# Performance work log

Hardware: AMD Instinct MI355X
Metric: run time of the kernel (lower is better)

## Reference

```python
import jax, jax.numpy as jnp
import numpy as np

N = 1_000_000
C = 64
H = Wd = 2048
EPS = 1e-5


def _build_neighbors(seed=0):
    """Active-site neighbor map for a 3x3 submanifold conv on an HxW grid.
    Returns int32 [N, 9]; entry = index of active neighbor site, or -1."""
    rng = np.random.default_rng(seed)
    flat = rng.permutation(H * Wd)[:N]            # unique active coords
    grid = np.full(H * Wd, -1, np.int64)
    grid[flat] = np.arange(N)
    ys, xs = flat // Wd, flat % Wd
    cols = []
    for dy in (-1, 0, 1):
        for dx in (-1, 0, 1):
            ny, nx = ys + dy, xs + dx
            valid = (ny >= 0) & (ny < H) & (nx >= 0) & (nx < Wd)
            nf = np.where(valid, np.clip(ny, 0, H - 1) * Wd + np.clip(nx, 0, Wd - 1), 0)
            nb = np.where(valid, grid[nf], -1)    # -1 also if neighbor inactive
            cols.append(nb)
    return np.stack(cols, axis=1).astype(np.int32)


def setup_inputs() -> dict:
    key = jax.random.key(0)
    k1, k2, k3 = jax.random.split(key, 3)
    scale = 1.0 / np.sqrt(9 * C)
    return {
        "features": jax.random.normal(k1, (N, C), jnp.float32),
        "neighbor": jnp.asarray(_build_neighbors()),
        "W1": jax.random.normal(k2, (9, C, C), jnp.float32) * scale,
        "gamma1": jnp.ones((C,), jnp.float32),
        "beta1": jnp.zeros((C,), jnp.float32),
        "W2": jax.random.normal(k3, (9, C, C), jnp.float32) * scale,
        "gamma2": jnp.ones((C,), jnp.float32),
        "beta2": jnp.zeros((C,), jnp.float32),
    }


def _subm_conv(f, W, neighbor):
    # gather -> per-tap GEMM -> accumulate (submanifold: outputs only at active sites)
    out = jnp.zeros_like(f)
    for k in range(9):
        idx = neighbor[:, k]
        mask = (idx >= 0)
        g = jnp.where(mask[:, None], f[jnp.maximum(idx, 0)], 0.0)  # [N, C]
        out = out + g @ W[k]
    return out


def _bn(f, gamma, beta):
    # BatchNorm1d over the active-site axis (training-mode batch statistics)
    m = f.mean(axis=0)
    v = f.var(axis=0)
    return (f - m) * jax.lax.rsqrt(v + EPS) * gamma + beta


def reference(features, neighbor, W1, gamma1, beta1, W2, gamma2, beta2):
    out = _subm_conv(features, W1, neighbor)
    out = jax.nn.relu(_bn(out, gamma1, beta1))
    out = _subm_conv(out, W2, neighbor)
    out = _bn(out, gamma2, beta2) + features
    return jax.nn.relu(out)
```

## Files before the change

kernel.cpp:

```cpp
#include <hip/hip_runtime.h>

#define NSITES 1000000
#define CCH 64
#define EPS_BN 1e-5f
#define INV_N (1.0f / 1000000.0f)

typedef __bf16 bf16x8 __attribute__((ext_vector_type(8)));
typedef float f32x4 __attribute__((ext_vector_type(4)));
typedef unsigned short ushort_t;

__device__ __forceinline__ unsigned short f2bf(float x) {
    __bf16 h = (__bf16)x;
    return __builtin_bit_cast(unsigned short, h);
}
__device__ __forceinline__ float bf2f(unsigned short u) {
    return (float)__builtin_bit_cast(__bf16, u);
}

__device__ __forceinline__ unsigned int actu32(unsigned int u, float a0, float b0,
                                               float a1, float b1) {
    float x0 = __builtin_bit_cast(float, u << 16);
    float x1 = __builtin_bit_cast(float, u & 0xffff0000u);
    float y0 = fmaxf(a0 * x0 + b0, 0.f);
    float y1 = fmaxf(a1 * x1 + b1, 0.f);
    return (unsigned int)f2bf(y0) | ((unsigned int)f2bf(y1) << 16);
}

__global__ void prep_kernel(const float* __restrict__ f, ushort_t* __restrict__ o,
                            const float* __restrict__ W1, const float* __restrict__ W2,
                            ushort_t* __restrict__ W1s, ushort_t* __restrict__ W2s,
                            float* __restrict__ stats, int total16) {
    int gtid = blockIdx.x * blockDim.x + threadIdx.x;
    if (gtid < 73728) {
        const float* Wg = W1;
        ushort_t* dst = W1s;
        int u = gtid;
        if (u >= 36864) { Wg = W2; dst = W2s; u -= 36864; }
        int j = u & 7;
        int lane = (u >> 3) & 63;
        int nt = (u >> 9) & 3;
        int kk = (u >> 11) & 1;
        int tap = u >> 12;
        int k = 32 * kk + 8 * (lane >> 4) + j;
        int n = 16 * nt + (lane & 15);
        dst[u] = f2bf(Wg[tap * 4096 + k * 64 + n]);
    } else if (gtid < 73984) {
        stats[gtid - 73728] = 0.f;
    } else if (gtid < 74016) {
        ((unsigned int*)(o + (size_t)NSITES * 64))[gtid - 73984] = 0u;
    }
    int stride = gridDim.x * blockDim.x;
    for (int i = gtid; i < total16; i += stride) {
        const float4* fp = (const float4*)(f + (size_t)i * 16);
        float4 v0 = fp[0];
        float4 v1 = fp[1];
        float4 v2 = fp[2];
        float4 v3 = fp[3];
        uint4 pa, pb;
        ushort_t* up = (ushort_t*)&pa;
        up[0] = f2bf(v0.x); up[1] = f2bf(v0.y); up[2] = f2bf(v0.z); up[3] = f2bf(v0.w);
        up[4] = f2bf(v1.x); up[5] = f2bf(v1.y); up[6] = f2bf(v1.z); up[7] = f2bf(v1.w);
        ushort_t* uq = (ushort_t*)&pb;
        uq[0] = f2bf(v2.x); uq[1] = f2bf(v2.y); uq[2] = f2bf(v2.z); uq[3] = f2bf(v2.w);
        uq[4] = f2bf(v3.x); uq[5] = f2bf(v3.y); uq[6] = f2bf(v3.z); uq[7] = f2bf(v3.w);
        uint4* op = (uint4*)(o + (size_t)i * 16);
        op[0] = pa;
        op[1] = pb;
    }
}

__device__ __forceinline__ void gatherA(const ushort_t* __restrict__ fin,
                                        const int (&idxr)[2][9], int t, int quad,
                                        uint4 (&dst)[2][2], int fallback) {
#pragma unroll
    for (int mt = 0; mt < 2; ++mt) {
        int id = idxr[mt][t];
        int r = (id < 0) ? fallback : id;
        const uint4* p = (const uint4*)(fin + ((size_t)r << 6) + (quad << 3));
        dst[mt][0] = p[0];
        dst[mt][1] = p[4];
    }
}

template <bool OUT_BF16, bool FUSE_ACT>
__global__ __launch_bounds__(256) void conv_kernel(
    const ushort_t* __restrict__ fin,
    const int* __restrict__ nbr,
    const ushort_t* __restrict__ Wsw,
    const float* __restrict__ p_sum, const float* __restrict__ p_sq,
    const float* __restrict__ p_gamma, const float* __restrict__ p_beta,
    ushort_t* __restrict__ out_bf, float* __restrict__ out_f,
    float* __restrict__ s_sum, float* __restrict__ s_sq) {

    __shared__ float bs_sum[64];
    __shared__ float bs_sq[64];
    __shared__ __align__(16) float s_a[64];
    __shared__ __align__(16) float s_b[64];

    const int tid  = threadIdx.x;
    const int wv   = tid >> 6;
    const int lane = tid & 63;
    const int quad = lane >> 4;
    const int l15  = lane & 15;
    const int sbase = blockIdx.x * 128 + wv * 32;

    if (tid < 64) {
        bs_sum[tid] = 0.f;
        bs_sq[tid] = 0.f;
        if constexpr (FUSE_ACT) {
            float m = p_sum[tid] * INV_N;
            float v = p_sq[tid] * INV_N - m * m;
            float s = p_gamma[tid] * rsqrtf(v + EPS_BN);
            s_a[tid] = s;
            s_b[tid] = p_beta[tid] - m * s;
        }
    }
    __syncthreads();

    float af[16], bfv[16];
    if constexpr (FUSE_ACT) {
#pragma unroll
        for (int j = 0; j < 8; ++j) {
            af[j]      = s_a[quad * 8 + j];
            af[8 + j]  = s_a[32 + quad * 8 + j];
            bfv[j]     = s_b[quad * 8 + j];
            bfv[8 + j] = s_b[32 + quad * 8 + j];
        }
    }

    int idxr[2][9];
#pragma unroll
    for (int mt = 0; mt < 2; ++mt) {
        int s = sbase + mt * 16 + l15;
        int sc = (s < NSITES) ? s : 0;
        bool sv = (s < NSITES);
#pragma unroll
        for (int t = 0; t < 9; ++t) {
            int id = nbr[(size_t)sc * 9 + t];
            idxr[mt][t] = sv ? id : -1;
        }
    }

    f32x4 acc[2][4];
#pragma unroll
    for (int mt = 0; mt < 2; ++mt)
#pragma unroll
        for (int nt = 0; nt < 4; ++nt) acc[mt][nt] = (f32x4){0.f, 0.f, 0.f, 0.f};

    constexpr int FB = FUSE_ACT ? 0 : NSITES;

    uint4 abuf[2][2][2];
    gatherA(fin, idxr, 0, quad, abuf[0], FB);

#pragma unroll
    for (int t = 0; t < 9; ++t) {
        bf16x8 B[2][4];
#pragma unroll
        for (int kk = 0; kk < 2; ++kk)
#pragma unroll
            for (int nt = 0; nt < 4; ++nt)
                B[kk][nt] = *(const bf16x8*)(Wsw + (size_t)(((t * 2 + kk) * 4 + nt) * 64 + lane) * 8);

        if (t < 8) gatherA(fin, idxr, t + 1, quad, abuf[(t + 1) & 1], FB);

        bf16x8 afr[2][2];
#pragma unroll
        for (int mt = 0; mt < 2; ++mt) {
            uint4 r0 = abuf[t & 1][mt][0];
            uint4 r1 = abuf[t & 1][mt][1];
            if constexpr (FUSE_ACT) {
                bool inv = idxr[mt][t] < 0;
                unsigned int* p0 = (unsigned int*)&r0;
                unsigned int* p1 = (unsigned int*)&r1;
#pragma unroll
                for (int p = 0; p < 4; ++p) {
                    unsigned int t0 = actu32(p0[p], af[2 * p], bfv[2 * p],
                                             af[2 * p + 1], bfv[2 * p + 1]);
                    unsigned int t1 = actu32(p1[p], af[8 + 2 * p], bfv[8 + 2 * p],
                                             af[8 + 2 * p + 1], bfv[8 + 2 * p + 1]);
                    p0[p] = inv ? 0u : t0;
                    p1[p] = inv ? 0u : t1;
                }
            }
            afr[mt][0] = __builtin_bit_cast(bf16x8, r0);
            afr[mt][1] = __builtin_bit_cast(bf16x8, r1);
        }

        __builtin_amdgcn_s_setprio(1);
#pragma unroll
        for (int mt = 0; mt < 2; ++mt) {
#pragma unroll
            for (int nt = 0; nt < 4; ++nt) {
                acc[mt][nt] = __builtin_amdgcn_mfma_f32_16x16x32_bf16(afr[mt][0], B[0][nt], acc[mt][nt], 0, 0, 0);
                acc[mt][nt] = __builtin_amdgcn_mfma_f32_16x16x32_bf16(afr[mt][1], B[1][nt], acc[mt][nt], 0, 0, 0);
            }
        }
        __builtin_amdgcn_s_setprio(0);
    }

    float ss[4] = {0.f, 0.f, 0.f, 0.f};
    float sq[4] = {0.f, 0.f, 0.f, 0.f};
#pragma unroll
    for (int mt = 0; mt < 2; ++mt)
#pragma unroll
        for (int nt = 0; nt < 4; ++nt)
#pragma unroll
            for (int r = 0; r < 4; ++r) {
                float v = acc[mt][nt][r];
                ss[nt] += v;
                sq[nt] += v * v;
            }
#pragma unroll
    for (int nt = 0; nt < 4; ++nt) {
        ss[nt] += __shfl_xor(ss[nt], 16);
        ss[nt] += __shfl_xor(ss[nt], 32);
        sq[nt] += __shfl_xor(sq[nt], 16);
        sq[nt] += __shfl_xor(sq[nt], 32);
    }
    if (lane < 16) {
#pragma unroll
        for (int nt = 0; nt < 4; ++nt) {
            atomicAdd(&bs_sum[nt * 16 + l15], ss[nt]);
            atomicAdd(&bs_sq[nt * 16 + l15], sq[nt]);
        }
    }

    if constexpr (OUT_BF16) {
        __shared__ ushort_t tr[4 * 32 * 72];
        ushort_t* w_tr = tr + wv * 32 * 72;
#pragma unroll
        for (int mt = 0; mt < 2; ++mt)
#pragma unroll
            for (int nt = 0; nt < 4; ++nt)
#pragma unroll
                for (int r = 0; r < 4; ++r)
                    w_tr[(mt * 16 + 4 * quad + r) * 72 + nt * 16 + l15] = f2bf(acc[mt][nt][r]);
        int site_s = lane >> 1;
        int half = lane & 1;
        int gs = sbase + site_s;
        if (gs < NSITES) {
#pragma unroll
            for (int c = 0; c < 4; ++c) {
                uint4 d = *(const uint4*)(w_tr + site_s * 72 + half * 32 + c * 8);
                *(uint4*)(out_bf + (size_t)gs * 64 + half * 32 + c * 8) = d;
            }
        }
    } else {
#pragma unroll
        for (int mt = 0; mt < 2; ++mt)
#pragma unroll
            for (int nt = 0; nt < 4; ++nt)
#pragma unroll
                for (int r = 0; r < 4; ++r) {
                    int site = sbase + mt * 16 + 4 * quad + r;
                    if (site < NSITES)
                        out_f[(size_t)site * 64 + nt * 16 + l15] = acc[mt][nt][r];
                }
    }

    __syncthreads();
    if (tid < 64) {
        atomicAdd(&s_sum[tid], bs_sum[tid]);
        atomicAdd(&s_sq[tid], bs_sq[tid]);
    }
}

__global__ void residual_kernel(float* __restrict__ out, const float* __restrict__ feat,
                                const float* __restrict__ sum2, const float* __restrict__ sq2,
                                const float* __restrict__ gamma2, const float* __restrict__ beta2,
                                int total8) {
    __shared__ __align__(16) float sa[64];
    __shared__ __align__(16) float sb[64];
    if (threadIdx.x < 64) {
        int c = threadIdx.x;
        float m = sum2[c] * INV_N;
        float v = sq2[c] * INV_N - m * m;
        float s = gamma2[c] * rsqrtf(v + EPS_BN);
        sa[c] = s;
        sb[c] = beta2[c] - m * s;
    }
    __syncthreads();
    int stride = gridDim.x * blockDim.x;
    for (int i = blockIdx.x * blockDim.x + threadIdx.x; i < total8; i += stride) {
        float4* op = (float4*)(out + (size_t)i * 8);
        const float4* fp = (const float4*)(feat + (size_t)i * 8);
        float4 h0 = op[0];
        float4 h1v = op[1];
        float4 f0 = fp[0];
        float4 f1 = fp[1];
        int c8 = (i & 7) * 8;
        float4 av0 = *(const float4*)&sa[c8];
        float4 av1 = *(const float4*)&sa[c8 + 4];
        float4 bv0 = *(const float4*)&sb[c8];
        float4 bv1 = *(const float4*)&sb[c8 + 4];
        float4 r0, r1;
        r0.x = fmaxf(av0.x * h0.x + bv0.x + f0.x, 0.f);
        r0.y = fmaxf(av0.y * h0.y + bv0.y + f0.y, 0.f);
        r0.z = fmaxf(av0.z * h0.z + bv0.z + f0.z, 0.f);
        r0.w = fmaxf(av0.w * h0.w + bv0.w + f0.w, 0.f);
        r1.x = fmaxf(av1.x * h1v.x + bv1.x + f1.x, 0.f);
        r1.y = fmaxf(av1.y * h1v.y + bv1.y + f1.y, 0.f);
        r1.z = fmaxf(av1.z * h1v.z + bv1.z + f1.z, 0.f);
        r1.w = fmaxf(av1.w * h1v.w + bv1.w + f1.w, 0.f);
        op[0] = r0;
        op[1] = r1;
    }
}

extern "C" void kernel_launch(void* const* d_in, const int* in_sizes, int n_in,
                              void* d_out, int out_size, void* d_ws, size_t ws_size,
                              hipStream_t stream) {
    const float* features = (const float*)d_in[0];
    const int* nbr        = (const int*)d_in[1];
    const float* W1       = (const float*)d_in[2];
    const float* gamma1   = (const float*)d_in[3];
    const float* beta1    = (const float*)d_in[4];
    const float* W2       = (const float*)d_in[5];
    const float* gamma2   = (const float*)d_in[6];
    const float* beta2    = (const float*)d_in[7];

    char* ws = (char*)d_ws;
    const size_t NB = (size_t)NSITES * CCH * sizeof(unsigned short);

    ushort_t* fbf = (ushort_t*)d_out;
    ushort_t* h1  = (ushort_t*)ws;
    size_t off = NB + 512;
    ushort_t* W1s = (ushort_t*)(ws + off);
    ushort_t* W2s = (ushort_t*)(ws + off + 147456);
    float* stats  = (float*)(ws + off + 294912);

    prep_kernel<<<8192, 256, 0, stream>>>(features, fbf, W1, W2, W1s, W2s, stats,
                                          NSITES * CCH / 16);

    const int nblk = (NSITES + 127) / 128;
    conv_kernel<true, false><<<nblk, 256, 0, stream>>>(
        fbf, nbr, W1s, nullptr, nullptr, nullptr, nullptr,
        h1, nullptr, stats + 0, stats + 64);

    conv_kernel<false, true><<<nblk, 256, 0, stream>>>(
        h1, nbr, W2s, stats + 0, stats + 64, gamma1, beta1,
        nullptr, (float*)d_out, stats + 128, stats + 192);

    residual_kernel<<<8192, 256, 0, stream>>>((float*)d_out, features,
                                              stats + 128, stats + 192, gamma2, beta2,
                                              NSITES * CCH / 8);
}
```

Before: 974.6 us.

## Fuse fp32-to-bf16 feature conversion into first conv gather

Drops the separate pass that converted input features to bf16. The first convolution now gathers fp32 neighbor rows directly and converts them to bf16 in registers, with invalid neighbors pointing at a zeroed row. This removes one full read and write of the feature tensor but doubles the bytes fetched by the random nine-tap gather in the first conv.

```diff
diff --git a/kernel.cpp b/kernel.cpp
--- a/kernel.cpp
+++ b/kernel.cpp
@@ -26,10 +26,16 @@
     return (unsigned int)f2bf(y0) | ((unsigned int)f2bf(y1) << 16);
 }
 
-__global__ void prep_kernel(const float* __restrict__ f, ushort_t* __restrict__ o,
-                            const float* __restrict__ W1, const float* __restrict__ W2,
+__device__ __forceinline__ bf16x8 cvt8(float4 a, float4 b) {
+    bf16x8 r;
+    r[0] = (__bf16)a.x; r[1] = (__bf16)a.y; r[2] = (__bf16)a.z; r[3] = (__bf16)a.w;
+    r[4] = (__bf16)b.x; r[5] = (__bf16)b.y; r[6] = (__bf16)b.z; r[7] = (__bf16)b.w;
+    return r;
+}
+
+__global__ void prep_kernel(const float* __restrict__ W1, const float* __restrict__ W2,
                             ushort_t* __restrict__ W1s, ushort_t* __restrict__ W2s,
-                            float* __restrict__ stats, int total16) {
+                            float* __restrict__ stats, float* __restrict__ fzero) {
     int gtid = blockIdx.x * blockDim.x + threadIdx.x;
     if (gtid < 73728) {
         const float* Wg = W1;
@@ -46,45 +52,45 @@
         dst[u] = f2bf(Wg[tap * 4096 + k * 64 + n]);
     } else if (gtid < 73984) {
         stats[gtid - 73728] = 0.f;
-    } else if (gtid < 74016) {
-        ((unsigned int*)(o + (size_t)NSITES * 64))[gtid - 73984] = 0u;
-    }
-    int stride = gridDim.x * blockDim.x;
-    for (int i = gtid; i < total16; i += stride) {
-        const float4* fp = (const float4*)(f + (size_t)i * 16);
-        float4 v0 = fp[0];
-        float4 v1 = fp[1];
-        float4 v2 = fp[2];
-        float4 v3 = fp[3];
-        uint4 pa, pb;
-        ushort_t* up = (ushort_t*)&pa;
-        up[0] = f2bf(v0.x); up[1] = f2bf(v0.y); up[2] = f2bf(v0.z); up[3] = f2bf(v0.w);
-        up[4] = f2bf(v1.x); up[5] = f2bf(v1.y); up[6] = f2bf(v1.z); up[7] = f2bf(v1.w);
-        ushort_t* uq = (ushort_t*)&pb;
-        uq[0] = f2bf(v2.x); uq[1] = f2bf(v2.y); uq[2] = f2bf(v2.z); uq[3] = f2bf(v2.w);
-        uq[4] = f2bf(v3.x); uq[5] = f2bf(v3.y); uq[6] = f2bf(v3.z); uq[7] = f2bf(v3.w);
-        uint4* op = (uint4*)(o + (size_t)i * 16);
-        op[0] = pa;
-        op[1] = pb;
+    } else if (gtid < 74048) {
+        fzero[gtid - 73984] = 0.f;
     }
 }
 
 __device__ __forceinline__ void gatherA(const ushort_t* __restrict__ fin,
                                         const int (&idxr)[2][9], int t, int quad,
-                                        uint4 (&dst)[2][2], int fallback) {
+                                        uint4 (&dst)[2][2]) {
 #pragma unroll
     for (int mt = 0; mt < 2; ++mt) {
         int id = idxr[mt][t];
-        int r = (id < 0) ? fallback : id;
+        int r = (id < 0) ? 0 : id;
         const uint4* p = (const uint4*)(fin + ((size_t)r << 6) + (quad << 3));
         dst[mt][0] = p[0];
         dst[mt][1] = p[4];
     }
 }
 
-template <bool OUT_BF16, bool FUSE_ACT>
+__device__ __forceinline__ void gatherAF32(const float* __restrict__ fin,
+                                           const float* __restrict__ zrow,
+                                           const int (&idxr)[2][9], int t, int quad,
+                                           float4 (&dst)[2][2][2]) {
+#pragma unroll
+    for (int mt = 0; mt < 2; ++mt) {
+        int id = idxr[mt][t];
+        const float* rowp = (id < 0) ? zrow : (fin + (size_t)id * 64);
+        const float4* p = (const float4*)rowp + quad * 2;
+        dst[mt][0][0] = p[0];
+        dst[mt][0][1] = p[1];
+        dst[mt][1][0] = p[8];
+        dst[mt][1][1] = p[9];
+    }
+}
+
+template <bool OUT_BF16, bool FUSE_ACT, bool IN_F32>
 __global__ __launch_bounds__(256) void conv_kernel(
-    const ushort_t* __restrict__ fin,
+    const ushort_t* __restrict__ fin_bf,
+    const float* __restrict__ fin_f32,
+    const float* __restrict__ zrow,
     const int* __restrict__ nbr,
     const ushort_t* __restrict__ Wsw,
     const float* __restrict__ p_sum, const float* __restrict__ p_sq,
@@ -147,10 +153,10 @@
 #pragma unroll
         for (int nt = 0; nt < 4; ++nt) acc[mt][nt] = (f32x4){0.f, 0.f, 0.f, 0.f};
 
-    constexpr int FB = FUSE_ACT ? 0 : NSITES;
-
     uint4 abuf[2][2][2];
-    gatherA(fin, idxr, 0, quad, abuf[0], FB);
+    float4 abufF[2][2][2][2];
+    if constexpr (IN_F32) gatherAF32(fin_f32, zrow, idxr, 0, quad, abufF[0]);
+    else                  gatherA(fin_bf, idxr, 0, quad, abuf[0]);
 
 #pragma unroll
     for (int t = 0; t < 9; ++t) {
@@ -161,29 +167,37 @@
             for (int nt = 0; nt < 4; ++nt)
                 B[kk][nt] = *(const bf16x8*)(Wsw + (size_t)(((t * 2 + kk) * 4 + nt) * 64 + lane) * 8);
 
-        if (t < 8) gatherA(fin, idxr, t + 1, quad, abuf[(t + 1) & 1], FB);
+        if (t < 8) {
+            if constexpr (IN_F32) gatherAF32(fin_f32, zrow, idxr, t + 1, quad, abufF[(t + 1) & 1]);
+            else                  gatherA(fin_bf, idxr, t + 1, quad, abuf[(t + 1) & 1]);
+        }
 
         bf16x8 afr[2][2];
 #pragma unroll
         for (int mt = 0; mt < 2; ++mt) {
-            uint4 r0 = abuf[t & 1][mt][0];
-            uint4 r1 = abuf[t & 1][mt][1];
-            if constexpr (FUSE_ACT) {
-                bool inv = idxr[mt][t] < 0;
-                unsigned int* p0 = (unsigned int*)&r0;
-                unsigned int* p1 = (unsigned int*)&r1;
-#pragma unroll
-                for (int p = 0; p < 4; ++p) {
-                    unsigned int t0 = actu32(p0[p], af[2 * p], bfv[2 * p],
-                                             af[2 * p + 1], bfv[2 * p + 1]);
-                    unsigned int t1 = actu32(p1[p], af[8 + 2 * p], bfv[8 + 2 * p],
-                                             af[8 + 2 * p + 1], bfv[8 + 2 * p + 1]);
-                    p0[p] = inv ? 0u : t0;
-                    p1[p] = inv ? 0u : t1;
+            if constexpr (IN_F32) {
+                afr[mt][0] = cvt8(abufF[t & 1][mt][0][0], abufF[t & 1][mt][0][1]);
+                afr[mt][1] = cvt8(abufF[t & 1][mt][1][0], abufF[t & 1][mt][1][1]);
+            } else {
+                uint4 r0 = abuf[t & 1][mt][0];
+                uint4 r1 = abuf[t & 1][mt][1];
+                if constexpr (FUSE_ACT) {
+                    bool inv = idxr[mt][t] < 0;
+                    unsigned int* p0 = (unsigned int*)&r0;
+                    unsigned int* p1 = (unsigned int*)&r1;
+#pragma unroll
+                    for (int p = 0; p < 4; ++p) {
+                        unsigned int t0 = actu32(p0[p], af[2 * p], bfv[2 * p],
+                                                 af[2 * p + 1], bfv[2 * p + 1]);
+                        unsigned int t1 = actu32(p1[p], af[8 + 2 * p], bfv[8 + 2 * p],
+                                                 af[8 + 2 * p + 1], bfv[8 + 2 * p + 1]);
+                        p0[p] = inv ? 0u : t0;
+                        p1[p] = inv ? 0u : t1;
+                    }
                 }
+                afr[mt][0] = __builtin_bit_cast(bf16x8, r0);
+                afr[mt][1] = __builtin_bit_cast(bf16x8, r1);
             }
-            afr[mt][0] = __builtin_bit_cast(bf16x8, r0);
-            afr[mt][1] = __builtin_bit_cast(bf16x8, r1);
         }
 
         __builtin_amdgcn_s_setprio(1);
@@ -322,23 +336,22 @@
     char* ws = (char*)d_ws;
     const size_t NB = (size_t)NSITES * CCH * sizeof(unsigned short);
 
-    ushort_t* fbf = (ushort_t*)d_out;
     ushort_t* h1  = (ushort_t*)ws;
     size_t off = NB + 512;
     ushort_t* W1s = (ushort_t*)(ws + off);
     ushort_t* W2s = (ushort_t*)(ws + off + 147456);
     float* stats  = (float*)(ws + off + 294912);
-
-    prep_kernel<<<8192, 256, 0, stream>>>(features, fbf, W1, W2, W1s, W2s, stats,
-                                          NSITES * CCH / 16);
+    float* fzero  = (float*)(ws + off + 294912 + 1024);
+
+    prep_kernel<<<290, 256, 0, stream>>>(W1, W2, W1s, W2s, stats, fzero);
 
     const int nblk = (NSITES + 127) / 128;
-    conv_kernel<true, false><<<nblk, 256, 0, stream>>>(
-        fbf, nbr, W1s, nullptr, nullptr, nullptr, nullptr,
+    conv_kernel<true, false, true><<<nblk, 256, 0, stream>>>(
+        nullptr, features, fzero, nbr, W1s, nullptr, nullptr, nullptr, nullptr,
         h1, nullptr, stats + 0, stats + 64);
 
-    conv_kernel<false, true><<<nblk, 256, 0, stream>>>(
-        h1, nbr, W2s, stats + 0, stats + 64, gamma1, beta1,
+    conv_kernel<false, true, false><<<nblk, 256, 0, stream>>>(
+        h1, nullptr, nullptr, nbr, W2s, stats + 0, stats + 64, gamma1, beta1,
         nullptr, (float*)d_out, stats + 128, stats + 192);
 
     residual_kernel<<<8192, 256, 0, stream>>>((float*)d_out, features,
```

Result: no change. 976.8 us (+0.2%).
